# Kernel optimization log

Measured on AMD Instinct MI355X. Metric: run time of the kernel, lower is better.

The kernel has to match this reference:

```python
import jax, jax.numpy as jnp
import numpy as np

NEG_SLOPE = 0.2  # PyG GATConv default negative_slope


def gat_conv(x, src, dst, W, a_src, a_dst, b, concat):
    """One PyG-style GATConv (eval mode, self-loops already added to src/dst).
    x: [N, Fin], W: [Fin, H*C], a_src/a_dst: [H, C], b: [H*C] or [C].
    """
    N = x.shape[0]
    H, C = a_src.shape
    h = (x @ W).reshape(N, H, C)                       # [N,H,C]
    alpha_s = jnp.sum(h * a_src, axis=-1)              # [N,H]
    alpha_d = jnp.sum(h * a_dst, axis=-1)              # [N,H]
    e = alpha_s[src] + alpha_d[dst]                    # [E,H]
    e = jax.nn.leaky_relu(e, NEG_SLOPE)
    # scatter-softmax over incoming edges of each destination node
    m = jax.ops.segment_max(e, dst, num_segments=N)    # [N,H]
    p = jnp.exp(e - m[dst])                            # [E,H]
    s = jax.ops.segment_sum(p, dst, num_segments=N)    # [N,H]
    alpha = p / s[dst]                                 # [E,H]
    msg = h[src] * alpha[:, :, None]                   # [E,H,C]
    out = jax.ops.segment_sum(msg, dst, num_segments=N)  # [N,H,C]
    out = out.reshape(N, H * C) if concat else out.mean(axis=1)
    return out + b


def setup_inputs() -> dict:
    key = jax.random.key(0)
    ks = jax.random.split(key, 12)
    N, E = 50000, 800000
    IN_C, HID, HEADS, OUT_C = 1, 32, 4, 1
    HW = HID * HEADS  # 128
    x = jax.random.normal(ks[0], (N, IN_C), dtype=jnp.float32)
    edge_index = jax.random.randint(ks[1], (2, E), 0, N, dtype=jnp.int64)
    g = 0.1
    inp = {
        "x": x,
        "edge_index": edge_index,
        "W1": jax.random.normal(ks[2], (IN_C, HW), dtype=jnp.float32) * g,
        "a_src1": jax.random.normal(ks[3], (HEADS, HID), dtype=jnp.float32) * g,
        "a_dst1": jax.random.normal(ks[4], (HEADS, HID), dtype=jnp.float32) * g,
        "b1": jnp.zeros((HW,), dtype=jnp.float32),
        "W2": jax.random.normal(ks[5], (HW, HW), dtype=jnp.float32) * g,
        "a_src2": jax.random.normal(ks[6], (HEADS, HID), dtype=jnp.float32) * g,
        "a_dst2": jax.random.normal(ks[7], (HEADS, HID), dtype=jnp.float32) * g,
        "b2": jnp.zeros((HW,), dtype=jnp.float32),
        "W3": jax.random.normal(ks[8], (HW, OUT_C), dtype=jnp.float32) * g,
        "a_src3": jax.random.normal(ks[9], (1, OUT_C), dtype=jnp.float32) * g,
        "a_dst3": jax.random.normal(ks[10], (1, OUT_C), dtype=jnp.float32) * g,
        "b3": jnp.zeros((OUT_C,), dtype=jnp.float32),
    }
    return inp


def reference(x, edge_index, W1, a_src1, a_dst1, b1, W2, a_src2, a_dst2, b2,
              W3, a_src3, a_dst3, b3):
    N = x.shape[0]
    loop = jnp.arange(N, dtype=edge_index.dtype)
    # PyG GATConv add_self_loops=True (each layer): add once, reused by all layers
    src = jnp.concatenate([edge_index[0], loop])
    dst = jnp.concatenate([edge_index[1], loop])
    h = gat_conv(x, src, dst, W1, a_src1, a_dst1, b1, concat=True)
    h = jax.nn.elu(h)  # dropout is identity in eval mode
    h = gat_conv(h, src, dst, W2, a_src2, a_dst2, b2, concat=True)
    h = jax.nn.elu(h)
    out = gat_conv(h, src, dst, W3, a_src3, a_dst3, b3, concat=False)
    return out
```

## Files before the change

kernel.cpp:

```cpp
#include <hip/hip_runtime.h>
#include <math.h>

#define NEG_SLOPE 0.2f

typedef _Float16 hv4 __attribute__((ext_vector_type(4)));
typedef _Float16 hv8 __attribute__((ext_vector_type(8)));

static __device__ __forceinline__ float leaky(float v){ return v > 0.f ? v : NEG_SLOPE * v; }
static __device__ __forceinline__ float eluf(float v){ return v > 0.f ? v : expm1f(v); }
static __device__ __forceinline__ float eluf_fast(float v){ return v > 0.f ? v : __expf(v) - 1.f; }

__global__ void __launch_bounds__(256) hist_k(const int* __restrict__ edst, int* __restrict__ deg,
                                              int Eg, int Etot, int N){
  const int slot = blockIdx.x & 7;
  const int lo = (int)(((long long)slot * N) >> 3);
  const int hi = (int)(((long long)(slot + 1) * N) >> 3);
  const int stride = (gridDim.x >> 3) * blockDim.x;
  for (int e = (blockIdx.x >> 3) * blockDim.x + threadIdx.x; e < Etot; e += stride){
    int d = (e < Eg) ? edst[e] : (e - Eg);
    if (d >= lo && d < hi) atomicAdd(&deg[d], 1);
  }
}

__global__ void __launch_bounds__(256) scatter_k(const int* __restrict__ esrc, const int* __restrict__ edst,
                                                 int* __restrict__ cursor, int* __restrict__ csr_src,
                                                 int Eg, int Etot, int N){
  const int slot = blockIdx.x & 7;
  const int lo = (int)(((long long)slot * N) >> 3);
  const int hi = (int)(((long long)(slot + 1) * N) >> 3);
  const int stride = (gridDim.x >> 3) * blockDim.x;
  for (int e = (blockIdx.x >> 3) * blockDim.x + threadIdx.x; e < Etot; e += stride){
    int s, d;
    if (e < Eg){ d = edst[e]; if (d < lo || d >= hi) continue; s = esrc[e]; }
    else { s = d = e - Eg; if (d < lo || d >= hi) continue; }
    int pos = atomicAdd(&cursor[d], 1);
    csr_src[pos] = s;
  }
}

__global__ void __launch_bounds__(256) scan_part_k(const int* __restrict__ deg,
                                                   int* __restrict__ bsum, int N){
  __shared__ int red[256];
  const int t = threadIdx.x;
  const int base = blockIdx.x * 2048;
  int sum = 0;
  #pragma unroll
  for (int i = 0; i < 8; ++i){
    int idx = base + t + i * 256;
    if (idx < N) sum += deg[idx];
  }
  red[t] = sum; __syncthreads();
  #pragma unroll
  for (int d = 128; d; d >>= 1){
    if (t < d) red[t] += red[t + d];
    __syncthreads();
  }
  if (t == 0) bsum[blockIdx.x] = red[0];
}

__global__ void scan_tops_k(const int* __restrict__ bsum, int* __restrict__ boff,
                            int* __restrict__ row, int nb, int N){
  int t = threadIdx.x;
  int v = (t < nb) ? bsum[t] : 0;
  int orig = v;
  #pragma unroll
  for (int off = 1; off < 64; off <<= 1){
    int u = __shfl_up(v, off, 64);
    if (t >= off) v += u;
  }
  if (t < nb) boff[t] = v - orig;
  if (t == nb - 1) row[N] = v;
}

__global__ void __launch_bounds__(256) scan_write_k(const int* __restrict__ deg,
                                                    const int* __restrict__ boff,
                                                    int* __restrict__ row, int* __restrict__ cursor, int N){
  __shared__ int sdeg[2048];
  __shared__ int tsum[256];
  const int t = threadIdx.x;
  const int base = blockIdx.x * 2048;
  for (int i = t; i < 2048; i += 256){
    int idx = base + i;
    sdeg[i] = (idx < N) ? deg[idx] : 0;
  }
  __syncthreads();
  const int off = t * 8;
  int sum = 0;
  #pragma unroll
  for (int i = 0; i < 8; ++i) sum += sdeg[off + i];
  tsum[t] = sum; __syncthreads();
  for (int d = 1; d < 256; d <<= 1){
    int v = (t >= d) ? tsum[t - d] : 0;
    __syncthreads();
    tsum[t] += v;
    __syncthreads();
  }
  int run = boff[blockIdx.x] + ((t == 0) ? 0 : tsum[t - 1]);
  #pragma unroll
  for (int i = 0; i < 8; ++i){
    int idx = base + off + i;
    if (idx < N){ row[idx] = run; cursor[idx] = run; run += sdeg[off + i]; }
  }
}

__global__ void dots1_k(const float* __restrict__ W1, const float* __restrict__ a_s,
                        const float* __restrict__ a_d, float* __restrict__ dAdD){
  int t = threadIdx.x;
  float ps = W1[t] * a_s[t];
  float pd = W1[t] * a_d[t];
  #pragma unroll
  for (int off = 16; off; off >>= 1){
    ps += __shfl_xor(ps, off, 32);
    pd += __shfl_xor(pd, off, 32);
  }
  if ((t & 31) == 0){ dAdD[t >> 5] = ps; dAdD[4 + (t >> 5)] = pd; }
}

__global__ void __launch_bounds__(256) r1_k(const int* __restrict__ row, const int* __restrict__ csr_src,
                                            const float* __restrict__ x, const float* __restrict__ dAdD,
                                            float4* __restrict__ r4, int N){
  int node = blockIdx.x * 32 + (threadIdx.x >> 3);
  if (node >= N) return;
  const int q = threadIdx.x & 7;
  const int start = row[node], end = row[node + 1];
  const float xd = x[node];
  float dA0 = dAdD[0], dA1 = dAdD[1], dA2 = dAdD[2], dA3 = dAdD[3];
  float e0d = xd * dAdD[4], e1d = xd * dAdD[5], e2d = xd * dAdD[6], e3d = xd * dAdD[7];

  float s0 = 0.f, s1 = 0.f, s2 = 0.f, s3 = 0.f;
  float t0 = 0.f, t1 = 0.f, t2 = 0.f, t3 = 0.f;
  for (int i = start + q; i < end; i += 8){
    float xs = x[csr_src[i]];
    float p0 = __expf(leaky(xs * dA0 + e0d));
    float p1 = __expf(leaky(xs * dA1 + e1d));
    float p2 = __expf(leaky(xs * dA2 + e2d));
    float p3 = __expf(leaky(xs * dA3 + e3d));
    s0 += p0; s1 += p1; s2 += p2; s3 += p3;
    t0 += p0 * xs; t1 += p1 * xs; t2 += p2 * xs; t3 += p3 * xs;
  }
  #pragma unroll
  for (int off = 4; off; off >>= 1){
    s0 += __shfl_xor(s0, off, 8); t0 += __shfl_xor(t0, off, 8);
    s1 += __shfl_xor(s1, off, 8); t1 += __shfl_xor(t1, off, 8);
    s2 += __shfl_xor(s2, off, 8); t2 += __shfl_xor(t2, off, 8);
    s3 += __shfl_xor(s3, off, 8); t3 += __shfl_xor(t3, off, 8);
  }
  if (q == 0) r4[node] = make_float4(t0 / s0, t1 / s1, t2 / s2, t3 / s3);
}

__global__ void __launch_bounds__(256) gemm2_k(const float4* __restrict__ r4,
                                               const float* __restrict__ W1f, const float* __restrict__ b1f,
                                               const float* __restrict__ W,
                                               const float* __restrict__ a_s, const float* __restrict__ a_d,
                                               _Float16* __restrict__ hh, float* __restrict__ as_, float* __restrict__ ad_,
                                               int N){
  __shared__ float sA[128][68];
  __shared__ _Float16 sW[2][16][128];
  const int t = threadIdx.x;
  const int n0 = blockIdx.x * 64;
  const int tx = t & 15, ty = t >> 4;
  const int c0 = tx * 8, r0 = ty * 4;

  const int wk = t >> 5;
  const int wq = t & 31;

  float4 rw0, rw1;
  auto gloadW = [&](int k0){
    rw0 = *(const float4*)&W[(size_t)(k0 + wk) * 128 + wq * 4];
    rw1 = *(const float4*)&W[(size_t)(k0 + wk + 8) * 128 + wq * 4];
  };
  auto sstoreW = [&](int buf){
    hv4 a = {(_Float16)rw0.x, (_Float16)rw0.y, (_Float16)rw0.z, (_Float16)rw0.w};
    hv4 b = {(_Float16)rw1.x, (_Float16)rw1.y, (_Float16)rw1.z, (_Float16)rw1.w};
    *(hv4*)&sW[buf][wk][wq * 4]     = a;
    *(hv4*)&sW[buf][wk + 8][wq * 4] = b;
  };

  {
    const int nl = t & 63, q = t >> 6;
    const int gn = n0 + nl;
    float r = 0.f;
    const bool valid = (gn < N);
    if (valid){
      float4 rv = r4[gn];
      r = (q == 0) ? rv.x : (q == 1) ? rv.y : (q == 2) ? rv.z : rv.w;
    }
    #pragma unroll
    for (int j = 0; j < 32; ++j){
      const int c = q * 32 + j;
      float v = W1f[c] * r + b1f[c];
      v = eluf_fast(v);
      sA[c][nl] = valid ? v : 0.f;
    }
  }

  float acc[4][8];
  #pragma unroll
  for (int r = 0; r < 4; ++r)
    #pragma unroll
    for (int c = 0; c < 8; ++c) acc[r][c] = 0.f;

  gloadW(0); sstoreW(0); __syncthreads();

  #pragma unroll 1
  for (int tile = 0; tile < 8; ++tile){
    const int buf = tile & 1;
    if (tile < 7) gloadW((tile + 1) * 16);
    #pragma unroll
    for (int k = 0; k < 16; ++k){
      float4 aa = *(const float4*)&sA[tile * 16 + k][r0];
      hv8 wh = *(const hv8*)&sW[buf][k][c0];
      float av[4] = {aa.x, aa.y, aa.z, aa.w};
      float wv[8];
      #pragma unroll
      for (int c = 0; c < 8; ++c) wv[c] = (float)wh[c];
      #pragma unroll
      for (int r = 0; r < 4; ++r)
        #pragma unroll
        for (int c = 0; c < 8; ++c) acc[r][c] += av[r] * wv[c];
    }
    if (tile < 7){ sstoreW(1 - buf); __syncthreads(); }
  }

  float asv[8], adv[8];
  #pragma unroll
  for (int c = 0; c < 8; ++c){ asv[c] = a_s[c0 + c]; adv[c] = a_d[c0 + c]; }

  const int hd  = tx >> 2;
  const int off = (tx & 3) * 8;

  #pragma unroll
  for (int r = 0; r < 4; ++r){
    int n = n0 + r0 + r;
    if (n >= N) continue;
    hv8 hv;
    #pragma unroll
    for (int c = 0; c < 8; ++c) hv[c] = (_Float16)acc[r][c];
    *(hv8*)&hh[((size_t)hd * N + n) * 32 + off] = hv;
    float ps = 0.f, pd = 0.f;
    #pragma unroll
    for (int c = 0; c < 8; ++c){ ps += acc[r][c] * asv[c]; pd += acc[r][c] * adv[c]; }
    ps += __shfl_xor(ps, 1); ps += __shfl_xor(ps, 2);
    pd += __shfl_xor(pd, 1); pd += __shfl_xor(pd, 2);
    if ((tx & 3) == 0){
      as_[(size_t)hd * N + n] = ps;
      ad_[(size_t)hd * N + n] = pd;
    }
  }
}

__global__ void __launch_bounds__(256) node_aggr2_k(const int* __restrict__ row, const int* __restrict__ csr_src,
                                                    const float* __restrict__ as_, const float* __restrict__ ad_,
                                                    const _Float16* __restrict__ hh, const float* __restrict__ b2,
                                                    const float* __restrict__ W3, float* __restrict__ h3, int N){
  const int slot   = blockIdx.x & 7;
  const int chunk  = blockIdx.x >> 3;
  const int head   = slot >> 1;
  const int parity = slot & 1;
  const int t  = threadIdx.x;
  const int nl = t >> 2;
  const int q  = t & 3;
  const int node = chunk * 128 + parity * 64 + nl;
  if (node >= N) return;
  const int start = row[node], end = row[node + 1];
  const float* __restrict__ ash = as_ + (size_t)head * N;
  const _Float16* __restrict__ hhh = hh + (size_t)head * N * 32 + q * 8;
  const float adv = ad_[(size_t)head * N + node];

  float s = 0.f;
  float acc[8] = {0.f, 0.f, 0.f, 0.f, 0.f, 0.f, 0.f, 0.f};
  int i = start;

  int pre = (4 - (start & 3)) & 3;
  if (pre > end - start) pre = end - start;
  for (int k = 0; k < pre; ++k, ++i){
    int src = csr_src[i];
    float p = __expf(leaky(ash[src] + adv));
    hv8 hv = *(const hv8*)&hhh[(size_t)src * 32];
    s += p;
    #pragma unroll
    for (int c = 0; c < 8; ++c) acc[c] += (float)hv[c] * p;
  }
  for (; i + 4 <= end; i += 4){
    int4 ia = *(const int4*)&csr_src[i];
    float a0 = ash[ia.x], a1 = ash[ia.y], a2 = ash[ia.z], a3 = ash[ia.w];
    hv8 h0 = *(const hv8*)&hhh[(size_t)ia.x * 32];
    hv8 h1 = *(const hv8*)&hhh[(size_t)ia.y * 32];
    hv8 h2 = *(const hv8*)&hhh[(size_t)ia.z * 32];
    hv8 h3v = *(const hv8*)&hhh[(size_t)ia.w * 32];
    float p0 = __expf(leaky(a0 + adv));
    float p1 = __expf(leaky(a1 + adv));
    float p2 = __expf(leaky(a2 + adv));
    float p3 = __expf(leaky(a3 + adv));
    s += (p0 + p1) + (p2 + p3);
    #pragma unroll
    for (int c = 0; c < 8; ++c)
      acc[c] += (float)h0[c]*p0 + (float)h1[c]*p1 + (float)h2[c]*p2 + (float)h3v[c]*p3;
  }
  for (; i < end; ++i){
    int src = csr_src[i];
    float p = __expf(leaky(ash[src] + adv));
    hv8 hv = *(const hv8*)&hhh[(size_t)src * 32];
    s += p;
    #pragma unroll
    for (int c = 0; c < 8; ++c) acc[c] += (float)hv[c] * p;
  }

  const float inv = 1.f / s;
  const int c0 = head * 32 + q * 8;
  float part = 0.f;
  #pragma unroll
  for (int c = 0; c < 8; ++c){
    float v = eluf(acc[c] * inv + b2[c0 + c]);
    part += v * W3[c0 + c];
  }
  part += __shfl_xor(part, 1, 4);
  part += __shfl_xor(part, 2, 4);
  if (q == 0) unsafeAtomicAdd(&h3[node], part);
}

__global__ void __launch_bounds__(256) node_aggr3_k(const int* __restrict__ row, const int* __restrict__ csr_src,
                                                    const float* __restrict__ h3,
                                                    const float* __restrict__ a_s3, const float* __restrict__ a_d3,
                                                    const float* __restrict__ b3,
                                                    float* __restrict__ out, int N){
  int node = blockIdx.x * 32 + (threadIdx.x >> 3);
  if (node >= N) return;
  int q = threadIdx.x & 7;
  int start = row[node], end = row[node + 1];
  const float a_s3v = a_s3[0];
  const float adv = a_d3[0] * h3[node];
  float s = 0.f, acc = 0.f;
  for (int i = start + q; i < end; i += 8){
    int src = csr_src[i];
    float hv = h3[src];
    float p = __expf(leaky(a_s3v * hv + adv));
    s += p; acc += hv * p;
  }
  #pragma unroll
  for (int off = 4; off; off >>= 1){
    s += __shfl_xor(s, off, 8);
    acc += __shfl_xor(acc, off, 8);
  }
  if (q == 0) out[node] = acc / s + b3[0];
}

extern "C" void kernel_launch(void* const* d_in, const int* in_sizes, int n_in,
                              void* d_out, int out_size, void* d_ws, size_t ws_size,
                              hipStream_t stream){
  const float* x   = (const float*)d_in[0];
  const int*   ei  = (const int*)  d_in[1];
  const float* W1  = (const float*)d_in[2];
  const float* as1 = (const float*)d_in[3];
  const float* ad1 = (const float*)d_in[4];
  const float* b1  = (const float*)d_in[5];
  const float* W2  = (const float*)d_in[6];
  const float* as2 = (const float*)d_in[7];
  const float* ad2 = (const float*)d_in[8];
  const float* b2  = (const float*)d_in[9];
  const float* W3  = (const float*)d_in[10];
  const float* as3 = (const float*)d_in[11];
  const float* ad3 = (const float*)d_in[12];
  const float* b3  = (const float*)d_in[13];

  const int N    = in_sizes[0];
  const int Eg   = in_sizes[1] / 2;
  const int Etot = Eg + N;
  const int* esrc = ei;
  const int* edst = ei + Eg;

  char* w = (char*)d_ws;
  auto carve = [&](size_t bytes)->char*{
    char* p = w; w += (bytes + 15) & ~size_t(15); return p;
  };
  _Float16* hbuf = (_Float16*)carve((size_t)N * 128 * 2);
  float* r4b    = (float*)carve((size_t)N * 4 * 4);
  float* asb    = (float*)carve((size_t)N * 4 * 4);
  float* adb    = (float*)carve((size_t)N * 4 * 4);
  float* h3b    = (float*)carve((size_t)N * 4);
  int*   deg    = (int*)  carve((size_t)N * 4);
  int*   rowp   = (int*)  carve((size_t)(N + 1) * 4);
  int*   cursor = (int*)  carve((size_t)N * 4);
  int*   csr_src= (int*)  carve((size_t)Etot * 4);
  float* dAdD   = (float*)carve(8 * 4);
  int*   bsum   = (int*)  carve(64 * 4);
  int*   boff   = (int*)  carve(64 * 4);

  const int B = 256;
  auto cdiv = [](int a, int b){ return (a + b - 1) / b; };
  const int nb = cdiv(N, 2048);

  hipMemsetAsync(deg, 0, (size_t)N * 4, stream);
  hipMemsetAsync(h3b, 0, (size_t)N * 4, stream);
  hist_k<<<128 * 8, B, 0, stream>>>(edst, deg, Eg, Etot, N);
  scan_part_k<<<nb, B, 0, stream>>>(deg, bsum, N);
  scan_tops_k<<<1, 64, 0, stream>>>(bsum, boff, rowp, nb, N);
  scan_write_k<<<nb, B, 0, stream>>>(deg, boff, rowp, cursor, N);
  scatter_k<<<128 * 8, B, 0, stream>>>(esrc, edst, cursor, csr_src, Eg, Etot, N);

  dots1_k<<<1, 128, 0, stream>>>(W1, as1, ad1, dAdD);
  r1_k<<<cdiv(N, 32), B, 0, stream>>>(rowp, csr_src, x, dAdD, (float4*)r4b, N);

  gemm2_k<<<cdiv(N, 64), B, 0, stream>>>((const float4*)r4b, W1, b1,
                                         W2, as2, ad2, hbuf, asb, adb, N);
  node_aggr2_k<<<cdiv(N, 128) * 8, B, 0, stream>>>(rowp, csr_src, asb, adb,
                                                   hbuf, b2, W3, h3b, N);

  node_aggr3_k<<<cdiv(N, 32), B, 0, stream>>>(rowp, csr_src, h3b, as3, ad3, b3, (float*)d_out, N);
}
```

Baseline: 276.0 us.

## Sort nodes by degree within blocks to balance per-wavefront edge work

The scan kernel now bins each 2048-node block's nodes by in-degree with a shared-memory histogram and prefix scan, and writes a local permutation. The three aggregation kernels use this permutation to pick nodes, so lanes in a wavefront handle nodes of similar degree and divergence from uneven loop lengths shrinks. The cost is extra shared-memory atomics and scans in scan_write_k, an extra indirection per node, and less coalesced per-node reads and writes in the aggregation kernels.

```diff
diff --git a/kernel.cpp b/kernel.cpp
--- a/kernel.cpp
+++ b/kernel.cpp
@@ -2,6 +2,7 @@
 #include <math.h>
 
 #define NEG_SLOPE 0.2f
+#define DEGBINS 512
 
 typedef _Float16 hv4 __attribute__((ext_vector_type(4)));
 typedef _Float16 hv8 __attribute__((ext_vector_type(8)));
@@ -74,11 +75,14 @@
 
 __global__ void __launch_bounds__(256) scan_write_k(const int* __restrict__ deg,
                                                     const int* __restrict__ boff,
-                                                    int* __restrict__ row, int* __restrict__ cursor, int N){
+                                                    int* __restrict__ row, int* __restrict__ cursor,
+                                                    int* __restrict__ perm, int N){
   __shared__ int sdeg[2048];
   __shared__ int tsum[256];
+  __shared__ int lb[DEGBINS];
   const int t = threadIdx.x;
   const int base = blockIdx.x * 2048;
+  for (int i = t; i < DEGBINS; i += 256) lb[i] = 0;
   for (int i = t; i < 2048; i += 256){
     int idx = base + i;
     sdeg[i] = (idx < N) ? deg[idx] : 0;
@@ -86,8 +90,14 @@
   __syncthreads();
   const int off = t * 8;
   int sum = 0;
-  #pragma unroll
-  for (int i = 0; i < 8; ++i) sum += sdeg[off + i];
+  int lrank[8]; int lbin[8];
+  #pragma unroll
+  for (int i = 0; i < 8; ++i){
+    int v = sdeg[off + i];
+    sum += v;
+    lbin[i] = v < DEGBINS ? v : DEGBINS - 1;
+    lrank[i] = (base + off + i < N) ? atomicAdd(&lb[lbin[i]], 1) : 0;
+  }
   tsum[t] = sum; __syncthreads();
   for (int d = 1; d < 256; d <<= 1){
     int v = (t >= d) ? tsum[t - d] : 0;
@@ -95,11 +105,23 @@
     tsum[t] += v;
     __syncthreads();
   }
+  for (int d = 1; d < DEGBINS; d <<= 1){
+    int v0 = (t >= d) ? lb[t - d] : 0;
+    int v1 = (t + 256 >= d) ? lb[t + 256 - d] : 0;
+    __syncthreads();
+    lb[t] += v0; lb[t + 256] += v1;
+    __syncthreads();
+  }
   int run = boff[blockIdx.x] + ((t == 0) ? 0 : tsum[t - 1]);
   #pragma unroll
   for (int i = 0; i < 8; ++i){
     int idx = base + off + i;
-    if (idx < N){ row[idx] = run; cursor[idx] = run; run += sdeg[off + i]; }
+    if (idx < N){
+      row[idx] = run; cursor[idx] = run; run += sdeg[off + i];
+      int b = lbin[i];
+      int lo = b ? lb[b - 1] : 0;
+      perm[base + lo + lrank[i]] = idx;
+    }
   }
 }
 
@@ -117,10 +139,12 @@
 }
 
 __global__ void __launch_bounds__(256) r1_k(const int* __restrict__ row, const int* __restrict__ csr_src,
+                                            const int* __restrict__ perm,
                                             const float* __restrict__ x, const float* __restrict__ dAdD,
                                             float4* __restrict__ r4, int N){
-  int node = blockIdx.x * 32 + (threadIdx.x >> 3);
-  if (node >= N) return;
+  int g = blockIdx.x * 32 + (threadIdx.x >> 3);
+  if (g >= N) return;
+  const int node = perm[g];
   const int q = threadIdx.x & 7;
   const int start = row[node], end = row[node + 1];
   const float xd = x[node];
@@ -250,6 +274,7 @@
 }
 
 __global__ void __launch_bounds__(256) node_aggr2_k(const int* __restrict__ row, const int* __restrict__ csr_src,
+                                                    const int* __restrict__ perm,
                                                     const float* __restrict__ as_, const float* __restrict__ ad_,
                                                     const _Float16* __restrict__ hh, const float* __restrict__ b2,
                                                     const float* __restrict__ W3, float* __restrict__ h3, int N){
@@ -260,8 +285,9 @@
   const int t  = threadIdx.x;
   const int nl = t >> 2;
   const int q  = t & 3;
-  const int node = chunk * 128 + parity * 64 + nl;
-  if (node >= N) return;
+  const int g = chunk * 128 + parity * 64 + nl;
+  if (g >= N) return;
+  const int node = perm[g];
   const int start = row[node], end = row[node + 1];
   const float* __restrict__ ash = as_ + (size_t)head * N;
   const _Float16* __restrict__ hhh = hh + (size_t)head * N * 32 + q * 8;
@@ -320,12 +346,14 @@
 }
 
 __global__ void __launch_bounds__(256) node_aggr3_k(const int* __restrict__ row, const int* __restrict__ csr_src,
+                                                    const int* __restrict__ perm,
                                                     const float* __restrict__ h3,
                                                     const float* __restrict__ a_s3, const float* __restrict__ a_d3,
                                                     const float* __restrict__ b3,
                                                     float* __restrict__ out, int N){
-  int node = blockIdx.x * 32 + (threadIdx.x >> 3);
-  if (node >= N) return;
+  int g = blockIdx.x * 32 + (threadIdx.x >> 3);
+  if (g >= N) return;
+  const int node = perm[g];
   int q = threadIdx.x & 7;
   int start = row[node], end = row[node + 1];
   const float a_s3v = a_s3[0];
@@ -382,6 +410,7 @@
   int*   rowp   = (int*)  carve((size_t)(N + 1) * 4);
   int*   cursor = (int*)  carve((size_t)N * 4);
   int*   csr_src= (int*)  carve((size_t)Etot * 4);
+  int*   perm   = (int*)  carve((size_t)N * 4);
   float* dAdD   = (float*)carve(8 * 4);
   int*   bsum   = (int*)  carve(64 * 4);
   int*   boff   = (int*)  carve(64 * 4);
@@ -395,16 +424,16 @@
   hist_k<<<128 * 8, B, 0, stream>>>(edst, deg, Eg, Etot, N);
   scan_part_k<<<nb, B, 0, stream>>>(deg, bsum, N);
   scan_tops_k<<<1, 64, 0, stream>>>(bsum, boff, rowp, nb, N);
-  scan_write_k<<<nb, B, 0, stream>>>(deg, boff, rowp, cursor, N);
+  scan_write_k<<<nb, B, 0, stream>>>(deg, boff, rowp, cursor, perm, N);
   scatter_k<<<128 * 8, B, 0, stream>>>(esrc, edst, cursor, csr_src, Eg, Etot, N);
 
   dots1_k<<<1, 128, 0, stream>>>(W1, as1, ad1, dAdD);
-  r1_k<<<cdiv(N, 32), B, 0, stream>>>(rowp, csr_src, x, dAdD, (float4*)r4b, N);
+  r1_k<<<cdiv(N, 32), B, 0, stream>>>(rowp, csr_src, perm, x, dAdD, (float4*)r4b, N);
 
   gemm2_k<<<cdiv(N, 64), B, 0, stream>>>((const float4*)r4b, W1, b1,
                                          W2, as2, ad2, hbuf, asb, adb, N);
-  node_aggr2_k<<<cdiv(N, 128) * 8, B, 0, stream>>>(rowp, csr_src, asb, adb,
+  node_aggr2_k<<<cdiv(N, 128) * 8, B, 0, stream>>>(rowp, csr_src, perm, asb, adb,
                                                    hbuf, b2, W3, h3b, N);
 
-  node_aggr3_k<<<cdiv(N, 32), B, 0, stream>>>(rowp, csr_src, h3b, as3, ad3, b3, (float*)d_out, N);
-}
+  node_aggr3_k<<<cdiv(N, 32), B, 0, stream>>>(rowp, csr_src, perm, h3b, as3, ad3, b3, (float*)d_out, N);
+}
```

After: 290.3 us. 5.2% more time.
